# Optimization experiments

Hardware: AMD Instinct MI355X
Metric: run time of the kernel (lower is better)

The kernel has to match this reference:

```python
import jax, jax.numpy as jnp
import numpy as np

BITS = 4
GROUP_SIZE = 128
INF, OUTF, TOKENS = 4096, 11008, 256


def setup_inputs() -> dict:
    key = jax.random.key(0)
    k1, k2, k3, k4, k5 = jax.random.split(key, 5)
    n_groups = INF // GROUP_SIZE  # 32
    x = jax.random.normal(k1, (TOKENS, INF), dtype=jnp.float32)
    qweight = jax.random.randint(k2, (INF // 32 * BITS, OUTF), 0, 2**31 - 1, dtype=jnp.int32)
    qzeros = jax.random.randint(k3, (n_groups, OUTF // 32 * BITS), 0, 2**31 - 1, dtype=jnp.int32)
    scales = jax.random.uniform(k4, (n_groups, OUTF), dtype=jnp.float32, minval=1e-3, maxval=2e-2)
    bias = jax.random.normal(k5, (OUTF,), dtype=jnp.float32)
    return {"x": x, "qweight": qweight, "qzeros": qzeros, "scales": scales, "bias": bias}


def _dequantize(qweight, qzeros, scales):
    """Unpack int4 nibbles and build the fp32 weight [infeatures, outfeatures]."""
    shifts = jnp.arange(0, 32, BITS, dtype=jnp.int32)  # [8]
    mask = (1 << BITS) - 1
    out_f = qweight.shape[1]
    # qweight row packs 8 consecutive in-features -> [K, O] int in [0, 15]
    w = ((qweight[:, None, :] >> shifts[None, :, None]) & mask).reshape(-1, out_f)
    # qzeros col packs 8 consecutive out-features; stored as (zero - 1)
    n_groups = qzeros.shape[0]
    z = (((qzeros[:, :, None] >> shifts[None, None, :]) & mask) + 1).reshape(n_groups, out_f)
    g_idx = jnp.arange(w.shape[0], dtype=jnp.int32) // GROUP_SIZE  # [K]
    return (w - z[g_idx]).astype(jnp.float32) * scales[g_idx]


def reference(x, qweight, qzeros, scales, bias):
    W = _dequantize(qweight, qzeros, scales)  # [infeatures, outfeatures]
    return x @ W + bias  # [tokens, outfeatures]
```

## Files before the change

### kernel.cpp

```cpp
#include <hip/hip_runtime.h>
#include <stdint.h>

#define TOKENS  256
#define INF     4096
#define OUTF    11008
#define NGROUPS 32
#define KSPLIT  2
#define PHK     128
#define NPH     ((INF / KSPLIT) / PHK)
#define NTH     256

typedef __attribute__((ext_vector_type(2))) _Float16 f16x2;
typedef __attribute__((ext_vector_type(8))) _Float16 f16x8;
typedef __attribute__((ext_vector_type(2))) __fp16   pkh2;
typedef __attribute__((ext_vector_type(4))) float    f32x4;

union U32H2 { uint32_t u; f16x2 h; };
union H8    { f16x2 h2[4]; f16x8 h8; };
union PK    { pkh2 p; f16x2 h; };

__device__ __forceinline__ void gl2lds16(const void* g, void* l) {
    __builtin_amdgcn_global_load_lds(
        (const __attribute__((address_space(1))) uint32_t*)g,
        (__attribute__((address_space(3))) uint32_t*)l, 16, 0, 0);
}

__global__ __launch_bounds__(NTH)
void prep(const float* __restrict__ x, _Float16* __restrict__ x16,
          const float* __restrict__ bias, float* __restrict__ out) {
    const int b = blockIdx.x;
    if (b < 512) {
        const int t   = b * NTH + threadIdx.x;
        const int row = t >> 9;
        const int c   = t & 511;
        const float* p = x + (size_t)row * INF + c * 8;
        f32x4 v0 = *(const f32x4*)p;
        f32x4 v1 = *(const f32x4*)(p + 4);
        H8 o; PK k0, k1, k2, k3;
        k0.p = __builtin_amdgcn_cvt_pkrtz(v0[0], v1[0]);
        k1.p = __builtin_amdgcn_cvt_pkrtz(v0[1], v1[1]);
        k2.p = __builtin_amdgcn_cvt_pkrtz(v0[2], v1[2]);
        k3.p = __builtin_amdgcn_cvt_pkrtz(v0[3], v1[3]);
        o.h2[0] = k0.h; o.h2[1] = k1.h; o.h2[2] = k2.h; o.h2[3] = k3.h;
        *(f16x8*)(x16 + (size_t)row * INF + c * 8) = o.h8;
    } else {
        const int t = (b - 512) * NTH + threadIdx.x;
        const int c = t % (OUTF / 4);
        const int r = t / (OUTF / 4);
        const f32x4 bv = ((const f32x4*)bias)[c];
        ((f32x4*)out)[(size_t)r * (OUTF / 4) + c] = bv;
    }
}

__global__ __launch_bounds__(NTH, 3)
void qlin_main(const _Float16* __restrict__ x16,
               const uint32_t* __restrict__ qweight,
               const uint32_t* __restrict__ qzeros,
               const float* __restrict__ scales,
               float* __restrict__ out)
{
    __shared__ alignas(16) _Float16 As[2][64 * PHK];

    const int tid = threadIdx.x;

    const int d  = blockIdx.x;
    const int cx = d & 7, kk = d >> 3;
    int strip, memb;
    if (kk < 80) { strip = cx * 10 + (kk >> 3); memb = kk & 7; }
    else         { const int t2 = ((kk - 80) << 3) | cx; strip = 80 + (t2 >> 3); memb = t2 & 7; }
    const int bx = strip;
    const int by = memb >> 1;
    const int ks = memb & 1;

    const int lane = tid & 63;
    const int quad = lane >> 4;
    const int l16  = lane & 15;
    const int wv   = tid >> 6;

    const int rowoff = tid >> 4;
    const int chk    = tid & 15;
    const int row0   = by * 64;
    const uint32_t aoff = (uint32_t)((row0 + rowoff) * (INF * 2)
                                     + ks * (INF / KSPLIT) * 2
                                     + ((chk ^ rowoff) & 15) * 16);
    const char* x16b = (const char*)x16;
    _Float16* ldsW = &As[0][0];
    const int ldsSlotBase = wv * 512;

    const int col0 = bx * 128 + wv * 32 + l16;
    const int col1 = col0 + 16;
    const int bOff0 = quad * OUTF + col0;
    const int bOff1 = quad * OUTF + col1;
    const int zsh   = (col0 & 7) * 4;
    const int qrow0 = ks * (INF / KSPLIT / 8);
    const int g0    = ks * (NGROUPS / KSPLIT);

    f32x4 acc[4][2];
#pragma unroll
    for (int mi = 0; mi < 4; ++mi)
#pragma unroll
        for (int nf = 0; nf < 2; ++nf)
            acc[mi][nf] = f32x4{0.f, 0.f, 0.f, 0.f};

    uint32_t Breg[4][8];
    float    sS[4][2];
    uint32_t qZ[4][2];

#define LOAD_B(SLOT, PN)                                                         \
    {                                                                            \
        const int gn_ = g0 + (PN);                                               \
        sS[SLOT][0] = scales[gn_ * OUTF + col0];                                 \
        sS[SLOT][1] = scales[gn_ * OUTF + col1];                                 \
        qZ[SLOT][0] = qzeros[gn_ * (OUTF / 8) + (col0 >> 3)];                    \
        qZ[SLOT][1] = qzeros[gn_ * (OUTF / 8) + (col1 >> 3)];                    \
        const uint32_t* qpb_ = qweight + (size_t)(qrow0 + (PN) * 16) * OUTF;     \
        _Pragma("unroll")                                                        \
        for (int s_ = 0; s_ < 4; ++s_) {                                         \
            Breg[SLOT][2 * s_ + 0] = qpb_[(size_t)(s_ * 4) * OUTF + bOff0];      \
            Breg[SLOT][2 * s_ + 1] = qpb_[(size_t)(s_ * 4) * OUTF + bOff1];      \
        }                                                                        \
    }

#pragma unroll
    for (int r = 0; r < 4; ++r)
        gl2lds16(x16b + aoff + r * 131072, ldsW + r * 2048 + ldsSlotBase);
    __builtin_amdgcn_sched_barrier(0);
    LOAD_B(0, 0)
    __builtin_amdgcn_sched_barrier(0);
    LOAD_B(1, 1)

#define PHASE_BODY(PAR, P, DO_A, DO_B, WAIT0)                                    \
    {                                                                            \
        __builtin_amdgcn_sched_barrier(0);                                       \
        if (WAIT0) { asm volatile("s_waitcnt vmcnt(0)" ::: "memory"); }          \
        else       { asm volatile("s_waitcnt vmcnt(12)" ::: "memory"); }         \
        __builtin_amdgcn_s_barrier();                                            \
        __builtin_amdgcn_sched_barrier(0);                                       \
        if (DO_A) {                                                              \
            const uint32_t pb = (uint32_t)(((P) + 1) * (PHK * 2));               \
            _Float16* ldsN = ldsW + (1 - ((PAR) & 1)) * 8192;                    \
            _Pragma("unroll")                                                    \
            for (int r = 0; r < 4; ++r)                                          \
                gl2lds16(x16b + aoff + r * 131072 + pb,                          \
                         ldsN + r * 2048 + ldsSlotBase);                         \
            __builtin_amdgcn_sched_barrier(0);        \
        }                                                                        \
        if (DO_B) {                                                              \
            LOAD_B(((PAR) + 2) & 3, (P) + 2)                                     \
        }                                                                        \
        f16x2 hs2[2], hz2[2];                                                    \
        _Pragma("unroll")                                                        \
        for (int nf = 0; nf < 2; ++nf) {                                         \
            const float s = sS[PAR][nf];                                         \
            const int   z = (int)((qZ[PAR][nf] >> zsh) & 15u) + 1025;            \
            const _Float16 hs = (_Float16)s;                                     \
            const _Float16 hz = (_Float16)(-(float)z);                           \
            hs2[nf] = f16x2{hs, hs};                                             \
            hz2[nf] = f16x2{hz, hz};                                             \
        }                                                                        \
        const _Float16* buf = ldsW + ((PAR) & 1) * 8192;                         \
        _Pragma("unroll")                                                        \
        for (int s = 0; s < 4; ++s) {                                            \
            f16x8 af[4];                                                         \
            _Pragma("unroll")                                                    \
            for (int mi = 0; mi < 4; ++mi) {                                     \
                const int m  = mi * 16 + l16;                                    \
                const int sc = ((s * 4 + quad) ^ l16) & 15;                      \
                af[mi] = *(const f16x8*)(buf + m * PHK + sc * 8);                \
            }                                                                    \
            _Pragma("unroll")                                                    \
            for (int nf = 0; nf < 2; ++nf) {                                     \
                const uint32_t q = Breg[PAR][2 * s + nf];                        \
                H8 b;                                                            \
                _Pragma("unroll")                                                \
                for (int j = 0; j < 4; ++j) {                                    \
                    U32H2 u;                                                     \
                    u.u = ((q >> (4 * j)) & 0x000F000Fu) | 0x64006400u;          \
                    b.h2[j] = (u.h + hz2[nf]) * hs2[nf];                         \
                }                                                                \
                __builtin_amdgcn_s_setprio(1);                                   \
                _Pragma("unroll")                                                \
                for (int mi = 0; mi < 4; ++mi)                                   \
                    acc[mi][nf] = __builtin_amdgcn_mfma_f32_16x16x32_f16(        \
                        af[mi], b.h8, acc[mi][nf], 0, 0, 0);                     \
                __builtin_amdgcn_s_setprio(0);                                   \
            }                                                                    \
        }                                                                        \
    }

#pragma unroll 1
    for (int pp = 0; pp < 3; ++pp) {
        const int pb4 = pp * 4;
        PHASE_BODY(0, pb4 + 0, true, true, false)
        PHASE_BODY(1, pb4 + 1, true, true, false)
        PHASE_BODY(2, pb4 + 2, true, true, false)
        PHASE_BODY(3, pb4 + 3, true, true, false)
    }
    PHASE_BODY(0, 12, true,  true,  false)
    PHASE_BODY(1, 13, true,  true,  false)
    PHASE_BODY(2, 14, true,  false, false)
    PHASE_BODY(3, 15, false, false, true)
#undef PHASE_BODY
#undef LOAD_B

#pragma unroll
    for (int nf = 0; nf < 2; ++nf) {
        const int col = (nf == 0) ? col0 : col1;
#pragma unroll
        for (int mi = 0; mi < 4; ++mi) {
            const int r0 = by * 64 + mi * 16 + quad * 4;
#pragma unroll
            for (int rg = 0; rg < 4; ++rg)
                unsafeAtomicAdd(&out[(size_t)(r0 + rg) * OUTF + col],
                                acc[mi][nf][rg]);
        }
    }
}

__global__ __launch_bounds__(NTH, 2)
void qlin_fb(const float* __restrict__ x,
             const uint32_t* __restrict__ qweight,
             const uint32_t* __restrict__ qzeros,
             const float* __restrict__ scales,
             const float* __restrict__ bias,
             float* __restrict__ out)
{
    __shared__ alignas(16) _Float16 Asb[64][40];
    __shared__ alignas(16) _Float16 Bsb[128][40];
    const int tid = threadIdx.x;
    const int bx = blockIdx.x, by = blockIdx.y;
    const int am = tid >> 2, ar = tid & 3;
    const float* xrow = x + (size_t)(by * 64 + am) * INF + ar * 8;
    const int bc = tid & 127, br = tid >> 7;
    const int bn = bx * 128 + bc;
    const int bswz = (bc >> 3) & 3;
    const int lane = tid & 63, quad = lane >> 4, l16 = lane & 15;
    const int wv = tid >> 6, wm = wv >> 1, wn = wv & 1;
    f32x4 acc[2][4];
#pragma unroll
    for (int i = 0; i < 2; ++i)
#pragma unroll
        for (int j = 0; j < 4; ++j) acc[i][j] = f32x4{0.f, 0.f, 0.f, 0.f};
    f32x4 pa0 = *(const f32x4*)(xrow + 0);
    f32x4 pa1 = *(const f32x4*)(xrow + 4);
    uint32_t pq0 = qweight[(size_t)br * OUTF + bn];
    uint32_t pq1 = qweight[(size_t)(br + 2) * OUTF + bn];
    for (int g = 0; g < NGROUPS; ++g) {
        const float s = scales[g * OUTF + bn];
        const uint32_t qzv = qzeros[g * (OUTF / 8) + (bn >> 3)];
        const int z = (int)((qzv >> (4 * (bn & 7))) & 15u) + 1;
        const _Float16 hs = (_Float16)s;
        const _Float16 hz = (_Float16)(-(float)(1024 + z));
        const f16x2 hs2 = {hs, hs}, hz2 = {hz, hz};
#pragma unroll
        for (int t4 = 0; t4 < 4; ++t4) {
            const int it = (g << 2) + t4;
            { H8 ah; PK p0, p1, p2, p3;
              p0.p = __builtin_amdgcn_cvt_pkrtz(pa0[0], pa1[0]);
              p1.p = __builtin_amdgcn_cvt_pkrtz(pa0[1], pa1[1]);
              p2.p = __builtin_amdgcn_cvt_pkrtz(pa0[2], pa1[2]);
              p3.p = __builtin_amdgcn_cvt_pkrtz(pa0[3], pa1[3]);
              ah.h2[0] = p0.h; ah.h2[1] = p1.h; ah.h2[2] = p2.h; ah.h2[3] = p3.h;
              *(f16x8*)&Asb[am][ar * 8] = ah.h8; }
            { const uint32_t qq[2] = {pq0, pq1};
#pragma unroll
              for (int rr = 0; rr < 2; ++rr) {
                  const int r = br + rr * 2; H8 bh;
#pragma unroll
                  for (int jp = 0; jp < 4; ++jp) {
                      U32H2 u; u.u = ((qq[rr] >> (4 * jp)) & 0x000F000Fu) | 0x64006400u;
                      bh.h2[jp] = (u.h + hz2) * hs2;
                  }
                  *(f16x8*)&Bsb[bc][(r ^ bswz) * 8] = bh.h8;
              } }
            __syncthreads();
            const int itn = (it < 127) ? it + 1 : 127;
            pa0 = *(const f32x4*)(xrow + itn * 32);
            pa1 = *(const f32x4*)(xrow + itn * 32 + 4);
            pq0 = qweight[(size_t)(itn * 4 + br) * OUTF + bn];
            pq1 = qweight[(size_t)(itn * 4 + br + 2) * OUTF + bn];
            f16x8 af[2], bf[4];
#pragma unroll
            for (int mi = 0; mi < 2; ++mi)
                af[mi] = *(const f16x8*)&Asb[wm * 32 + mi * 16 + l16][quad * 8];
#pragma unroll
            for (int ni = 0; ni < 4; ++ni) {
                const int c = wn * 64 + ni * 16 + l16;
                bf[ni] = *(const f16x8*)&Bsb[c][(quad ^ ((c >> 3) & 3)) * 8];
            }
#pragma unroll
            for (int mi = 0; mi < 2; ++mi)
#pragma unroll
                for (int ni = 0; ni < 4; ++ni)
                    acc[mi][ni] = __builtin_amdgcn_mfma_f32_16x16x32_f16(
                        af[mi], bf[ni], acc[mi][ni], 0, 0, 0);
            __syncthreads();
        }
    }
#pragma unroll
    for (int ni = 0; ni < 4; ++ni) {
        const int col = bx * 128 + wn * 64 + ni * 16 + l16;
        const float bv = bias[col];
#pragma unroll
        for (int mi = 0; mi < 2; ++mi) {
            const int row0 = by * 64 + wm * 32 + mi * 16 + quad * 4;
#pragma unroll
            for (int rg = 0; rg < 4; ++rg)
                out[(size_t)(row0 + rg) * OUTF + col] = acc[mi][ni][rg] + bv;
        }
    }
}

extern "C" void kernel_launch(void* const* d_in, const int* in_sizes, int n_in,
                              void* d_out, int out_size, void* d_ws, size_t ws_size,
                              hipStream_t stream) {
    const float*    xx = (const float*)d_in[0];
    const uint32_t* qw = (const uint32_t*)d_in[1];
    const uint32_t* qz = (const uint32_t*)d_in[2];
    const float*    sc = (const float*)d_in[3];
    const float*    bs = (const float*)d_in[4];
    float* out = (float*)d_out;

    const size_t x16_bytes = (size_t)TOKENS * INF * sizeof(_Float16);
    if (ws_size >= x16_bytes) {
        _Float16* x16 = (_Float16*)d_ws;
        prep<<<512 + (TOKENS * OUTF / 4) / NTH, NTH, 0, stream>>>(xx, x16, bs, out);
        qlin_main<<<(OUTF / 128) * (TOKENS / 64) * KSPLIT, NTH, 0, stream>>>(
            x16, qw, qz, sc, out);
    } else {
        dim3 grid(OUTF / 128, TOKENS / 64);
        qlin_fb<<<grid, NTH, 0, stream>>>(xx, qw, qz, sc, bs, out);
    }
}
```

Before: 119.9 us.

## Stagger k-phase start per block with wraparound to spread memory traffic

Each block now begins its k-loop at a phase offset derived from its group member index and wraps modulo 16, so blocks sharing a strip read different x and qweight rows at the same moment. The tail phases are made uniform: every phase issues A and B prefetches, with a final vmcnt(0) wait before the atomic adds. The aim is to reduce simultaneous hits on the same cache lines and DRAM channels. The cost is wasted wraparound prefetches at the end and extra index arithmetic.

Result: slower. 123.7 us (+3.1%).

```diff
diff --git a/kernel.cpp b/kernel.cpp
--- a/kernel.cpp
+++ b/kernel.cpp
@@ -71,6 +71,7 @@
     const int bx = strip;
     const int by = memb >> 1;
     const int ks = memb & 1;
+    const int pstart = memb * 2;
 
     const int lane = tid & 63;
     const int quad = lane >> 4;
@@ -106,14 +107,27 @@
     float    sS[4][2];
     uint32_t qZ[4][2];
 
-#define LOAD_B(SLOT, PN)                                                         \
+    int kpA = pstart;
+    int kpB = pstart;
+
+#define LOAD_A(BUF)                                                              \
     {                                                                            \
-        const int gn_ = g0 + (PN);                                               \
+        const uint32_t pb_ = (uint32_t)(kpA * (PHK * 2));                        \
+        _Float16* ldsN = ldsW + (BUF) * 8192;                                    \
+        _Pragma("unroll")                                                        \
+        for (int r = 0; r < 4; ++r)                                              \
+            gl2lds16(x16b + aoff + r * 131072 + pb_,                             \
+                     ldsN + r * 2048 + ldsSlotBase);                             \
+    }
+
+#define LOAD_B(SLOT)                                                             \
+    {                                                                            \
+        const int gn_ = g0 + kpB;                                                \
         sS[SLOT][0] = scales[gn_ * OUTF + col0];                                 \
         sS[SLOT][1] = scales[gn_ * OUTF + col1];                                 \
         qZ[SLOT][0] = qzeros[gn_ * (OUTF / 8) + (col0 >> 3)];                    \
         qZ[SLOT][1] = qzeros[gn_ * (OUTF / 8) + (col1 >> 3)];                    \
-        const uint32_t* qpb_ = qweight + (size_t)(qrow0 + (PN) * 16) * OUTF;     \
+        const uint32_t* qpb_ = qweight + (size_t)(qrow0 + kpB * 16) * OUTF;      \
         _Pragma("unroll")                                                        \
         for (int s_ = 0; s_ < 4; ++s_) {                                         \
             Breg[SLOT][2 * s_ + 0] = qpb_[(size_t)(s_ * 4) * OUTF + bOff0];      \
@@ -121,44 +135,37 @@
         }                                                                        \
     }
 
-#pragma unroll
-    for (int r = 0; r < 4; ++r)
-        gl2lds16(x16b + aoff + r * 131072, ldsW + r * 2048 + ldsSlotBase);
+    LOAD_A(0)
+    kpA = (kpA + 1) & 15;
     __builtin_amdgcn_sched_barrier(0);
-    LOAD_B(0, 0)
+    LOAD_B(0)
+    kpB = (kpB + 1) & 15;
     __builtin_amdgcn_sched_barrier(0);
-    LOAD_B(1, 1)
-
-#define PHASE_BODY(PAR, P, DO_A, DO_B, WAIT0)                                    \
+    LOAD_B(1)
+    kpB = (kpB + 1) & 15;
+
+#define PHASE_BODY(PAR, SLOT)                                                    \
     {                                                                            \
         __builtin_amdgcn_sched_barrier(0);                                       \
-        if (WAIT0) { asm volatile("s_waitcnt vmcnt(0)" ::: "memory"); }          \
-        else       { asm volatile("s_waitcnt vmcnt(12)" ::: "memory"); }         \
+        asm volatile("s_waitcnt vmcnt(12)" ::: "memory");                        \
         __builtin_amdgcn_s_barrier();                                            \
         __builtin_amdgcn_sched_barrier(0);                                       \
-        if (DO_A) {                                                              \
-            const uint32_t pb = (uint32_t)(((P) + 1) * (PHK * 2));               \
-            _Float16* ldsN = ldsW + (1 - ((PAR) & 1)) * 8192;                    \
-            _Pragma("unroll")                                                    \
-            for (int r = 0; r < 4; ++r)                                          \
-                gl2lds16(x16b + aoff + r * 131072 + pb,                          \
-                         ldsN + r * 2048 + ldsSlotBase);                         \
-            __builtin_amdgcn_sched_barrier(0);        \
-        }                                                                        \
-        if (DO_B) {                                                              \
-            LOAD_B(((PAR) + 2) & 3, (P) + 2)                                     \
-        }                                                                        \
+        LOAD_A(1 - (PAR))                                                        \
+        kpA = (kpA + 1) & 15;                                                    \
+        __builtin_amdgcn_sched_barrier(0);               \
+        LOAD_B(((SLOT) + 2) & 3)                                                 \
+        kpB = (kpB + 1) & 15;                                                    \
         f16x2 hs2[2], hz2[2];                                                    \
         _Pragma("unroll")                                                        \
         for (int nf = 0; nf < 2; ++nf) {                                         \
-            const float s = sS[PAR][nf];                                         \
-            const int   z = (int)((qZ[PAR][nf] >> zsh) & 15u) + 1025;            \
+            const float s = sS[SLOT][nf];                                        \
+            const int   z = (int)((qZ[SLOT][nf] >> zsh) & 15u) + 1025;           \
             const _Float16 hs = (_Float16)s;                                     \
             const _Float16 hz = (_Float16)(-(float)z);                           \
             hs2[nf] = f16x2{hs, hs};                                             \
             hz2[nf] = f16x2{hz, hz};                                             \
         }                                                                        \
-        const _Float16* buf = ldsW + ((PAR) & 1) * 8192;                         \
+        const _Float16* buf = ldsW + (PAR) * 8192;                               \
         _Pragma("unroll")                                                        \
         for (int s = 0; s < 4; ++s) {                                            \
             f16x8 af[4];                                                         \
@@ -170,7 +177,7 @@
             }                                                                    \
             _Pragma("unroll")                                                    \
             for (int nf = 0; nf < 2; ++nf) {                                     \
-                const uint32_t q = Breg[PAR][2 * s + nf];                        \
+                const uint32_t q = Breg[SLOT][2 * s + nf];                       \
                 H8 b;                                                            \
                 _Pragma("unroll")                                                \
                 for (int j = 0; j < 4; ++j) {                                    \
@@ -189,19 +196,17 @@
     }
 
 #pragma unroll 1
-    for (int pp = 0; pp < 3; ++pp) {
-        const int pb4 = pp * 4;
-        PHASE_BODY(0, pb4 + 0, true, true, false)
-        PHASE_BODY(1, pb4 + 1, true, true, false)
-        PHASE_BODY(2, pb4 + 2, true, true, false)
-        PHASE_BODY(3, pb4 + 3, true, true, false)
-    }
-    PHASE_BODY(0, 12, true,  true,  false)
-    PHASE_BODY(1, 13, true,  true,  false)
-    PHASE_BODY(2, 14, true,  false, false)
-    PHASE_BODY(3, 15, false, false, true)
+    for (int pp = 0; pp < 4; ++pp) {
+        PHASE_BODY(0, 0)
+        PHASE_BODY(1, 1)
+        PHASE_BODY(0, 2)
+        PHASE_BODY(1, 3)
+    }
 #undef PHASE_BODY
+#undef LOAD_A
 #undef LOAD_B
+
+    asm volatile("s_waitcnt vmcnt(0)" ::: "memory");
 
 #pragma unroll
     for (int nf = 0; nf < 2; ++nf) {
```
